# Kernel optimization log

Measured on AMD Instinct MI355X. Metric: run time of the kernel, lower is better.

## Reference

```python
import jax, jax.numpy as jnp
import numpy as np

GAMMA = 1.0
CONNECTIVITY_WEIGHT = 0.001


def setup_inputs() -> dict:
    key = jax.random.key(0)
    k1, k2 = jax.random.split(key)
    B, C, P, L = 65536, 2, 41, 4
    logits = jax.random.normal(k1, (B, C, P, L), dtype=jnp.float32)
    targets = jax.random.randint(k2, (B, P, L), 0, C, dtype=jnp.int64)
    return {"logits": logits, "targets": targets}


def compute_boundary_weights(labels, alpha=GAMMA):
    # labels: [B, P, L] int -> float boundary weights [B, P, L]
    beta = alpha * 0.5
    lab = labels.astype(jnp.float32)
    diff1 = jnp.abs(lab[:, 1:, :] - lab[:, :-1, :])   # [B, P-1, L]
    diff2 = jnp.abs(lab[:, 2:, :] - lab[:, :-2, :])   # [B, P-2, L]
    w = jnp.zeros_like(lab)
    w = w.at[:, 1:, :].add(alpha * diff1)
    w = w.at[:, :-1, :].add(alpha * diff1)
    w = w.at[:, 2:, :].add(beta * diff2)
    w = w.at[:, :-2, :].add(beta * diff2)
    return w + 1.0


def reference(logits, targets):
    # logits: [B, C, P, L], targets: [B, P, L]
    # Cross-entropy over class dim (axis=1), reduction='none'
    logp = jax.nn.log_softmax(logits, axis=1)                      # [B, C, P, L]
    loss_ce = -jnp.take_along_axis(logp, targets[:, None, :, :], axis=1)[:, 0]  # [B, P, L]

    weights = compute_boundary_weights(targets, GAMMA)
    weighted_loss_ce = loss_ce * weights

    # Connectivity: 1 where consecutive predicted classes differ (point 0 -> 0)
    pred = jnp.argmax(logits, axis=1)                              # [B, P, L]
    diff = (pred[:, 1:, :] != pred[:, :-1, :]).astype(loss_ce.dtype)
    connectivity = jnp.concatenate(
        [jnp.zeros_like(diff[:, :1, :]), diff], axis=1)            # [B, P, L]

    total = weighted_loss_ce + CONNECTIVITY_WEIGHT * connectivity
    return jnp.mean(total)
```

## Files before the change

kernel.cpp:

```cpp
#include <hip/hip_runtime.h>

constexpr int B   = 65536;
constexpr int P   = 41;
constexpr int CPL4 = 82;
constexpr int NTH  = B * P;
constexpr int GS   = 41 * 16384;
constexpr int ITER = 4;
constexpr int NBLK = GS / 256;
constexpr float INV_N = 1.0f / (float)(B * P * 4);
constexpr float CW    = 0.001f;

__device__ __forceinline__ int pack_tgt(int4 v) {
    return (v.x & 1) | ((v.y & 1) << 1) | ((v.z & 1) << 2) | ((v.w & 1) << 3);
}
__device__ __forceinline__ int pack_pred(float4 c0, float4 c1) {
    return (c1.x > c0.x ? 1 : 0) | (c1.y > c0.y ? 2 : 0) |
           (c1.z > c0.z ? 4 : 0) | (c1.w > c0.w ? 8 : 0);
}

__global__ __launch_bounds__(256)
void lace_partial_kernel(const float4* __restrict__ lg4,
                         const int4*   __restrict__ tg4,
                         float*        __restrict__ partial)
{
    const int tid  = blockIdx.x * 256 + threadIdx.x;
    const int lane = threadIdx.x & 63;

    int b = tid / P;
    const int p = tid - b * P;

    const bool hm1 = (p >= 1), hp1 = (p <= P - 2);
    const bool hm2 = (p >= 2), hp2 = (p <= P - 3);
    const bool im1 = (lane >= 1), ip1 = (lane <= 62);
    const bool im2 = (lane >= 2), ip2 = (lane <= 61);

    float sum = 0.0f;
    int t = tid;

    #pragma unroll
    for (int k = 0; k < ITER; ++k) {
        const int f4 = b * CPL4 + p;
        float4 a0 = lg4[f4];
        float4 a1 = lg4[f4 + P];
        int4   tc = tg4[t];

        int tp = pack_tgt(tc);
        int pp = pack_pred(a0, a1);

        int tm1 = __shfl_up  (tp, 1, 64);
        int tP1 = __shfl_down(tp, 1, 64);
        int tm2 = __shfl_up  (tp, 2, 64);
        int tP2 = __shfl_down(tp, 2, 64);
        int pm  = __shfl_up  (pp, 1, 64);

        if (hm1 && !im1) {
            tm1 = pack_tgt(tg4[t - 1]);
            pm  = pack_pred(lg4[f4 - 1], lg4[f4 + P - 1]);
        }
        if (hp1 && !ip1) tP1 = pack_tgt(tg4[t + 1]);
        if (hm2 && !im2) tm2 = pack_tgt(tg4[t - 2]);
        if (hp2 && !ip2) tP2 = pack_tgt(tg4[t + 2]);

        const int xm1 = hm1 ? (tp ^ tm1) & 0xF : 0;
        const int xp1 = hp1 ? (tp ^ tP1) & 0xF : 0;
        const int xm2 = hm2 ? (tp ^ tm2) & 0xF : 0;
        const int xp2 = hp2 ? (tp ^ tP2) & 0xF : 0;

        const float* A0 = (const float*)&a0;
        const float* A1 = (const float*)&a1;

        #pragma unroll
        for (int l = 0; l < 4; ++l) {
            float d  = A1[l] - A0[l];
            float ad = fabsf(d);
            float g  = __logf(1.0f + __expf(-ad));
            float sd = ((tp >> l) & 1) ? -d : d;
            float ce = fmaxf(sd, 0.0f) + g;

            float w = 1.0f
                    + (float)(((xm1 >> l) & 1) + ((xp1 >> l) & 1))
                    + 0.5f * (float)(((xm2 >> l) & 1) + ((xp2 >> l) & 1));
            sum += ce * w;
        }

        if (hm1) sum += CW * (float)__popc((pp ^ pm) & 0xF);

        t += GS;
        b += 16384;
    }

    #pragma unroll
    for (int off = 32; off > 0; off >>= 1)
        sum += __shfl_down(sum, off, 64);

    __shared__ float wsum[4];
    int wid = threadIdx.x >> 6;
    if (lane == 0) wsum[wid] = sum;
    __syncthreads();
    if (threadIdx.x == 0)
        partial[blockIdx.x] = wsum[0] + wsum[1] + wsum[2] + wsum[3];
}

__global__ __launch_bounds__(1024)
void lace_reduce_kernel(const float* __restrict__ partial,
                        float*       __restrict__ out)
{
    float s = 0.0f;
    for (int i = threadIdx.x; i < NBLK; i += 1024)
        s += partial[i];

    #pragma unroll
    for (int off = 32; off > 0; off >>= 1)
        s += __shfl_down(s, off, 64);

    __shared__ float wsum[16];
    int lane = threadIdx.x & 63;
    int wid  = threadIdx.x >> 6;
    if (lane == 0) wsum[wid] = s;
    __syncthreads();
    if (threadIdx.x == 0) {
        float total = 0.0f;
        #pragma unroll
        for (int i = 0; i < 16; ++i) total += wsum[i];
        out[0] = total * INV_N;
    }
}

extern "C" void kernel_launch(void* const* d_in, const int* in_sizes, int n_in,
                              void* d_out, int out_size, void* d_ws, size_t ws_size,
                              hipStream_t stream) {
    const float4* lg4 = (const float4*)d_in[0];
    const int4*   tg4 = (const int4*)d_in[1];
    float* out     = (float*)d_out;
    float* partial = (float*)d_ws;

    lace_partial_kernel<<<NBLK, 256, 0, stream>>>(lg4, tg4, partial);
    lace_reduce_kernel<<<1, 1024, 0, stream>>>(partial, out);
}
```

Before: 168.2 us.

## Assign four consecutive points per thread instead of shuffles across lanes

```diff
diff --git a/kernel.cpp b/kernel.cpp
--- a/kernel.cpp
+++ b/kernel.cpp
@@ -1,12 +1,10 @@
 #include <hip/hip_runtime.h>
 
-constexpr int B   = 65536;
-constexpr int P   = 41;
-constexpr int CPL4 = 82;
-constexpr int NTH  = B * P;
-constexpr int GS   = 41 * 16384;
-constexpr int ITER = 4;
-constexpr int NBLK = GS / 256;
+constexpr int B    = 65536;
+constexpr int P    = 41;
+constexpr int NQ   = 11;
+constexpr int NTHR = B * NQ;
+constexpr int NBLK = NTHR / 256;
 constexpr float INV_N = 1.0f / (float)(B * P * 4);
 constexpr float CW    = 0.001f;
 
@@ -23,70 +21,73 @@
                          const int4*   __restrict__ tg4,
                          float*        __restrict__ partial)
 {
-    const int tid  = blockIdx.x * 256 + threadIdx.x;
-    const int lane = threadIdx.x & 63;
+    const int tid = blockIdx.x * 256 + threadIdx.x;
+    const int b   = tid / NQ;
+    const int q   = tid - b * NQ;
+    const int p0  = q * 4;
 
-    int b = tid / P;
-    const int p = tid - b * P;
+    const int lbase = b * 82 + p0;
+    const int tbase = b * 41 + p0;
 
-    const bool hm1 = (p >= 1), hp1 = (p <= P - 2);
-    const bool hm2 = (p >= 2), hp2 = (p <= P - 3);
-    const bool im1 = (lane >= 1), ip1 = (lane <= 62);
-    const bool im2 = (lane >= 2), ip2 = (lane <= 61);
+    float4 c0v[4], c1v[4];
+    int4   tv[4];
+    #pragma unroll
+    for (int j = 0; j < 4; ++j) {
+        const int cl = (p0 + j <= 40) ? j : 0;
+        c0v[j] = lg4[lbase + cl];
+        c1v[j] = lg4[lbase + 41 + cl];
+        tv[j]  = tg4[tbase + cl];
+    }
+
+    int tm1b = 0, tm2b = 0, tp1b = 0, tp2b = 0, pmb = 0;
+    if (p0 >= 1) {
+        tm1b = pack_tgt(tg4[tbase - 1]);
+        tm2b = pack_tgt(tg4[tbase - 2]);
+        pmb  = pack_pred(lg4[lbase - 1], lg4[lbase + 40]);
+    }
+    if (p0 + 4 <= 40) tp1b = pack_tgt(tg4[tbase + 4]);
+    if (p0 + 5 <= 40) tp2b = pack_tgt(tg4[tbase + 5]);
+
+    int tb[4], pb[4];
+    #pragma unroll
+    for (int j = 0; j < 4; ++j) {
+        tb[j] = pack_tgt(tv[j]);
+        pb[j] = pack_pred(c0v[j], c1v[j]);
+    }
 
     float sum = 0.0f;
-    int t = tid;
+    #pragma unroll
+    for (int j = 0; j < 4; ++j) {
+        if (j == 0 || p0 + j <= 40) {
+            const int p  = p0 + j;
+            const int tp = tb[j];
+            const int prev1 = (j >= 1) ? tb[j-1] : tm1b;
+            const int prev2 = (j >= 2) ? tb[j-2] : ((j == 1) ? tm1b : tm2b);
+            const int next1 = (j <= 2) ? tb[j+1] : tp1b;
+            const int next2 = (j <= 1) ? tb[j+2] : ((j == 2) ? tp1b : tp2b);
+            const int prevp = (j >= 1) ? pb[j-1] : pmb;
 
-    #pragma unroll
-    for (int k = 0; k < ITER; ++k) {
-        const int f4 = b * CPL4 + p;
-        float4 a0 = lg4[f4];
-        float4 a1 = lg4[f4 + P];
-        int4   tc = tg4[t];
+            const int xm1 = (p >= 1)  ? (tp ^ prev1) & 0xF : 0;
+            const int xm2 = (p >= 2)  ? (tp ^ prev2) & 0xF : 0;
+            const int xp1 = (p <= 39) ? (tp ^ next1) & 0xF : 0;
+            const int xp2 = (p <= 38) ? (tp ^ next2) & 0xF : 0;
 
-        int tp = pack_tgt(tc);
-        int pp = pack_pred(a0, a1);
-
-        int tm1 = __shfl_up  (tp, 1, 64);
-        int tP1 = __shfl_down(tp, 1, 64);
-        int tm2 = __shfl_up  (tp, 2, 64);
-        int tP2 = __shfl_down(tp, 2, 64);
-        int pm  = __shfl_up  (pp, 1, 64);
-
-        if (hm1 && !im1) {
-            tm1 = pack_tgt(tg4[t - 1]);
-            pm  = pack_pred(lg4[f4 - 1], lg4[f4 + P - 1]);
+            const float* A0 = (const float*)&c0v[j];
+            const float* A1 = (const float*)&c1v[j];
+            #pragma unroll
+            for (int l = 0; l < 4; ++l) {
+                float d  = A1[l] - A0[l];
+                float g  = __logf(1.0f + __expf(-fabsf(d)));
+                float sd = ((tp >> l) & 1) ? -d : d;
+                float ce = fmaxf(sd, 0.0f) + g;
+                float w  = 1.0f
+                         + (float)(((xm1 >> l) & 1) + ((xp1 >> l) & 1))
+                         + 0.5f * (float)(((xm2 >> l) & 1) + ((xp2 >> l) & 1));
+                sum += ce * w;
+            }
+            if (p >= 1)
+                sum += CW * (float)__popc((pb[j] ^ prevp) & 0xF);
         }
-        if (hp1 && !ip1) tP1 = pack_tgt(tg4[t + 1]);
-        if (hm2 && !im2) tm2 = pack_tgt(tg4[t - 2]);
-        if (hp2 && !ip2) tP2 = pack_tgt(tg4[t + 2]);
-
-        const int xm1 = hm1 ? (tp ^ tm1) & 0xF : 0;
-        const int xp1 = hp1 ? (tp ^ tP1) & 0xF : 0;
-        const int xm2 = hm2 ? (tp ^ tm2) & 0xF : 0;
-        const int xp2 = hp2 ? (tp ^ tP2) & 0xF : 0;
-
-        const float* A0 = (const float*)&a0;
-        const float* A1 = (const float*)&a1;
-
-        #pragma unroll
-        for (int l = 0; l < 4; ++l) {
-            float d  = A1[l] - A0[l];
-            float ad = fabsf(d);
-            float g  = __logf(1.0f + __expf(-ad));
-            float sd = ((tp >> l) & 1) ? -d : d;
-            float ce = fmaxf(sd, 0.0f) + g;
-
-            float w = 1.0f
-                    + (float)(((xm1 >> l) & 1) + ((xp1 >> l) & 1))
-                    + 0.5f * (float)(((xm2 >> l) & 1) + ((xp2 >> l) & 1));
-            sum += ce * w;
-        }
-
-        if (hm1) sum += CW * (float)__popc((pp ^ pm) & 0xF);
-
-        t += GS;
-        b += 16384;
     }
 
     #pragma unroll
@@ -94,7 +95,8 @@
         sum += __shfl_down(sum, off, 64);
 
     __shared__ float wsum[4];
-    int wid = threadIdx.x >> 6;
+    const int lane = threadIdx.x & 63;
+    const int wid  = threadIdx.x >> 6;
     if (lane == 0) wsum[wid] = sum;
     __syncthreads();
     if (threadIdx.x == 0)
@@ -114,8 +116,8 @@
         s += __shfl_down(s, off, 64);
 
     __shared__ float wsum[16];
-    int lane = threadIdx.x & 63;
-    int wid  = threadIdx.x >> 6;
+    const int lane = threadIdx.x & 63;
+    const int wid  = threadIdx.x >> 6;
     if (lane == 0) wsum[wid] = s;
     __syncthreads();
     if (threadIdx.x == 0) {
```

Result: faster. 160.9 us (-4.4%).

## Replace wave shuffles with direct neighbor loads, one point per thread

Applied to the files above, without the earlier changes.

```diff
diff --git a/kernel.cpp b/kernel.cpp
--- a/kernel.cpp
+++ b/kernel.cpp
@@ -1,21 +1,28 @@
 #include <hip/hip_runtime.h>
 
-constexpr int B   = 65536;
-constexpr int P   = 41;
-constexpr int CPL4 = 82;
+constexpr int B    = 65536;
+constexpr int P    = 41;
 constexpr int NTH  = B * P;
-constexpr int GS   = 41 * 16384;
-constexpr int ITER = 4;
-constexpr int NBLK = GS / 256;
+constexpr int NBLK = NTH / 256;
 constexpr float INV_N = 1.0f / (float)(B * P * 4);
 constexpr float CW    = 0.001f;
 
-__device__ __forceinline__ int pack_tgt(int4 v) {
-    return (v.x & 1) | ((v.y & 1) << 1) | ((v.z & 1) << 2) | ((v.w & 1) << 3);
-}
-__device__ __forceinline__ int pack_pred(float4 c0, float4 c1) {
-    return (c1.x > c0.x ? 1 : 0) | (c1.y > c0.y ? 2 : 0) |
-           (c1.z > c0.z ? 4 : 0) | (c1.w > c0.w ? 8 : 0);
+__device__ __forceinline__ float comp1(float l0, float l1, float q0, float q1,
+                                       int tx, int am1, int ap1, int am2, int ap2)
+{
+    float d  = l1 - l0;
+    float g  = __logf(1.0f + __expf(-fabsf(d)));
+    float ft = (float)tx;
+    float sd = d * fmaf(-2.0f, ft, 1.0f);
+    float ce = fmaxf(sd, 0.0f) + g;
+
+    int   x1 = (tx ^ am1) + (tx ^ ap1);
+    int   x2 = (tx ^ am2) + (tx ^ ap2);
+    float w  = fmaf(0.5f, (float)x2, 1.0f + (float)x1);
+
+    float dm   = q1 - q0;
+    float conn = ((d > 0.0f) != (dm > 0.0f)) ? CW : 0.0f;
+    return fmaf(ce, w, conn);
 }
 
 __global__ __launch_bounds__(256)
@@ -23,78 +30,41 @@
                          const int4*   __restrict__ tg4,
                          float*        __restrict__ partial)
 {
-    const int tid  = blockIdx.x * 256 + threadIdx.x;
-    const int lane = threadIdx.x & 63;
+    const int t = blockIdx.x * 256 + threadIdx.x;
+    const int b = t / P;
+    const int p = t - b * P;
 
-    int b = tid / P;
-    const int p = tid - b * P;
+    const int pm1 = (p >= 1) ? p - 1 : p;
+    const int pp1 = (p <= P - 2) ? p + 1 : p;
+    const int pm2 = (p >= 2) ? p - 2 : p;
+    const int pp2 = (p <= P - 3) ? p + 2 : p;
 
-    const bool hm1 = (p >= 1), hp1 = (p <= P - 2);
-    const bool hm2 = (p >= 2), hp2 = (p <= P - 3);
-    const bool im1 = (lane >= 1), ip1 = (lane <= 62);
-    const bool im2 = (lane >= 2), ip2 = (lane <= 61);
+    const int f4 = b * 82 + p;
+    const int fm = b * 82 + pm1;
+    const int tb = t - p;
 
-    float sum = 0.0f;
-    int t = tid;
+    float4 a0 = lg4[f4];
+    float4 a1 = lg4[f4 + 41];
+    float4 q0 = lg4[fm];
+    float4 q1 = lg4[fm + 41];
+    int4   tc = tg4[t];
+    int4   nA = tg4[tb + pm1];
+    int4   nB = tg4[tb + pp1];
+    int4   nC = tg4[tb + pm2];
+    int4   nD = tg4[tb + pp2];
 
-    #pragma unroll
-    for (int k = 0; k < ITER; ++k) {
-        const int f4 = b * CPL4 + p;
-        float4 a0 = lg4[f4];
-        float4 a1 = lg4[f4 + P];
-        int4   tc = tg4[t];
-
-        int tp = pack_tgt(tc);
-        int pp = pack_pred(a0, a1);
-
-        int tm1 = __shfl_up  (tp, 1, 64);
-        int tP1 = __shfl_down(tp, 1, 64);
-        int tm2 = __shfl_up  (tp, 2, 64);
-        int tP2 = __shfl_down(tp, 2, 64);
-        int pm  = __shfl_up  (pp, 1, 64);
-
-        if (hm1 && !im1) {
-            tm1 = pack_tgt(tg4[t - 1]);
-            pm  = pack_pred(lg4[f4 - 1], lg4[f4 + P - 1]);
-        }
-        if (hp1 && !ip1) tP1 = pack_tgt(tg4[t + 1]);
-        if (hm2 && !im2) tm2 = pack_tgt(tg4[t - 2]);
-        if (hp2 && !ip2) tP2 = pack_tgt(tg4[t + 2]);
-
-        const int xm1 = hm1 ? (tp ^ tm1) & 0xF : 0;
-        const int xp1 = hp1 ? (tp ^ tP1) & 0xF : 0;
-        const int xm2 = hm2 ? (tp ^ tm2) & 0xF : 0;
-        const int xp2 = hp2 ? (tp ^ tP2) & 0xF : 0;
-
-        const float* A0 = (const float*)&a0;
-        const float* A1 = (const float*)&a1;
-
-        #pragma unroll
-        for (int l = 0; l < 4; ++l) {
-            float d  = A1[l] - A0[l];
-            float ad = fabsf(d);
-            float g  = __logf(1.0f + __expf(-ad));
-            float sd = ((tp >> l) & 1) ? -d : d;
-            float ce = fmaxf(sd, 0.0f) + g;
-
-            float w = 1.0f
-                    + (float)(((xm1 >> l) & 1) + ((xp1 >> l) & 1))
-                    + 0.5f * (float)(((xm2 >> l) & 1) + ((xp2 >> l) & 1));
-            sum += ce * w;
-        }
-
-        if (hm1) sum += CW * (float)__popc((pp ^ pm) & 0xF);
-
-        t += GS;
-        b += 16384;
-    }
+    float sum = comp1(a0.x, a1.x, q0.x, q1.x, tc.x, nA.x, nB.x, nC.x, nD.x)
+              + comp1(a0.y, a1.y, q0.y, q1.y, tc.y, nA.y, nB.y, nC.y, nD.y)
+              + comp1(a0.z, a1.z, q0.z, q1.z, tc.z, nA.z, nB.z, nC.z, nD.z)
+              + comp1(a0.w, a1.w, q0.w, q1.w, tc.w, nA.w, nB.w, nC.w, nD.w);
 
     #pragma unroll
     for (int off = 32; off > 0; off >>= 1)
         sum += __shfl_down(sum, off, 64);
 
     __shared__ float wsum[4];
-    int wid = threadIdx.x >> 6;
+    const int lane = threadIdx.x & 63;
+    const int wid  = threadIdx.x >> 6;
     if (lane == 0) wsum[wid] = sum;
     __syncthreads();
     if (threadIdx.x == 0)
@@ -114,8 +84,8 @@
         s += __shfl_down(s, off, 64);
 
     __shared__ float wsum[16];
-    int lane = threadIdx.x & 63;
-    int wid  = threadIdx.x >> 6;
+    const int lane = threadIdx.x & 63;
+    const int wid  = threadIdx.x >> 6;
     if (lane == 0) wsum[wid] = s;
     __syncthreads();
     if (threadIdx.x == 0) {
```

Measured after the change: 156.4 us, median of 2. 7.0% less time.
